# Optimization experiments

Measured on AMD Instinct MI355X. Metric: run time of the kernel, lower is better.

Reference implementation:

```python
import jax, jax.numpy as jnp
import numpy as np

VOCA = 30000
EMB = 128
REGION = 7
RADIUS = REGION // 2
NUM_CLASSES = 20
MAX_LEN = 512
ENTIRE = MAX_LEN - 2 * RADIUS
BATCH = 64


def _uniform(k, shape, lo=-0.01, hi=0.01):
    return jax.random.uniform(k, shape, dtype=jnp.float32, minval=lo, maxval=hi)


def _xavier(k, shape):
    fan_out, fan_in = shape
    lim = float(np.sqrt(6.0 / (fan_in + fan_out)))
    return jax.random.uniform(k, shape, dtype=jnp.float32, minval=-lim, maxval=lim)


def setup_inputs() -> dict:
    key = jax.random.key(0)
    ks = jax.random.split(key, 8)
    train_input = jax.random.randint(ks[0], (BATCH, MAX_LEN), 0, VOCA, dtype=jnp.int64)
    # padding_idx=0 -> row 0 is zero in both tables
    emb_region = _uniform(ks[1], (VOCA, REGION * EMB)).at[0].set(0.0)
    emb_word = _uniform(ks[2], (VOCA, EMB)).at[0].set(0.0)
    W_inter = _uniform(ks[3], (NUM_CLASSES, EMB))
    W_agg1 = _xavier(ks[4], (MAX_LEN * 2, ENTIRE))
    b_agg1 = jnp.zeros((MAX_LEN * 2,), jnp.float32)
    W_agg2 = _xavier(ks[5], (1, MAX_LEN * 2))
    b_agg2 = jnp.zeros((1,), jnp.float32)
    return {
        "train_input": train_input,
        "emb_region": emb_region,
        "emb_word": emb_word,
        "W_inter": W_inter,
        "W_agg1": W_agg1,
        "b_agg1": b_agg1,
        "W_agg2": W_agg2,
        "b_agg2": b_agg2,
    }


def reference(train_input, emb_region, emb_word, W_inter, W_agg1, b_agg1, W_agg2, b_agg2):
    B, L = train_input.shape
    entire = L - 2 * RADIUS
    # region embedding of center tokens -> [B, entire, REGION, EMB]
    trimed = train_input[:, RADIUS:L - RADIUS]
    K = emb_region[trimed].reshape(B, entire, REGION, EMB)
    # sliding-window gather of context tokens -> [B, entire, REGION]
    pos = jnp.arange(entire)[:, None] + jnp.arange(REGION)[None, :]
    E = emb_word[train_input[:, pos]]  # [B, entire, REGION, EMB]
    # elementwise interaction, max over region, relu
    inter = jax.nn.relu(jnp.max(E * K, axis=2))  # [B, entire, EMB]
    # per-class word-level scores -> [B, C, entire]
    inter = jnp.einsum("bne,ce->bcn", inter, W_inter)
    # aggregation MLP over the 'entire' axis (dropout inactive at eval)
    h = jax.nn.relu(inter @ W_agg1.T + b_agg1)  # [B, C, 2*MAX_LEN]
    agreg = (h @ W_agg2.T + b_agg2)[..., 0]  # [B, C]
    prob = jax.nn.softmax(agreg, axis=1)
    class_ = jnp.argmax(prob, axis=1)
    return agreg, prob, class_
```

## Files before the change

### kernel.cpp

```cpp
#include <hip/hip_runtime.h>
#include <math.h>

#define BATCH   64
#define MAXLEN  512
#define EMB     128
#define REGION  7
#define RADIUS  3
#define ENTIRE  506
#define NCLS    20
#define AGG1    1024
#define TILE_N  16
#define ICP     512

__global__ __launch_bounds__(256) void k1_inter(
        const int*   __restrict__ ti,
        const float* __restrict__ embR,
        const float* __restrict__ embW,
        const float* __restrict__ Wint,
        float*       __restrict__ interC) {
    __shared__ float wordbuf[TILE_N + 6][EMB];
    __shared__ float interL[TILE_N][EMB + 1];
    __shared__ float wl[NCLS][EMB + 2];
    __shared__ int   wid[TILE_N + 6];

    const int b   = blockIdx.y;
    const int n0  = blockIdx.x * TILE_N;
    const int np  = min(TILE_N, ENTIRE - n0);
    const int tid = threadIdx.x;

    if (tid < TILE_N + 6) {
        int r = tid;
        wid[r] = (n0 + r < MAXLEN) ? ti[b * MAXLEN + n0 + r] : 0;
    }
    for (int idx = tid; idx < NCLS * EMB; idx += 256) {
        int c = idx >> 7, e = idx & 127;
        wl[c][e] = Wint[idx];
    }
    __syncthreads();

    for (int idx = tid; idx < (TILE_N + 6) * EMB; idx += 256) {
        int r = idx >> 7, e = idx & 127;
        wordbuf[r][e] = embW[(long)wid[r] * EMB + e];
    }
    __syncthreads();

    for (int pp = 0; pp < TILE_N; pp += 2) {
        int p = pp + (tid >> 7);
        int e = tid & 127;
        if (p < np) {
            long t = wid[p + RADIUS];
            const float* kr = embR + t * (REGION * EMB) + e;
            float m = -INFINITY;
            #pragma unroll
            for (int j = 0; j < REGION; ++j) {
                float ew = wordbuf[p + j][e];
                float kk = kr[(long)j * EMB];
                m = fmaxf(m, ew * kk);
            }
            interL[p][e] = fmaxf(m, 0.f);
        }
    }
    __syncthreads();

    for (int out = tid; out < NCLS * TILE_N; out += 256) {
        int c = out >> 4;
        int p = out & 15;
        int n = n0 + p;
        if (p < np) {
            float s = 0.f;
            #pragma unroll 8
            for (int e = 0; e < EMB; ++e)
                s += interL[p][e] * wl[c][e];
            interC[((long)b * NCLS + c) * ICP + n] = s;
        }
    }
}

__global__ __launch_bounds__(256) void k2_gemm(
        const float* __restrict__ interC,
        const float* __restrict__ Wagg1,
        const float* __restrict__ bagg1,
        float*       __restrict__ h) {
    const int n  = blockIdx.x * 256 + threadIdx.x;
    const int m0 = blockIdx.y * 16;

    float acc[16];
    #pragma unroll
    for (int i = 0; i < 16; ++i) acc[i] = 0.f;

    const float2* w2  = (const float2*)Wagg1 + (long)n * (ENTIRE / 2);
    const float*  icb = interC + (long)m0 * ICP;

    for (int kc = 0; kc < 126; ++kc) {
        float2 wa = w2[kc * 2];
        float2 wb = w2[kc * 2 + 1];
        #pragma unroll
        for (int mm = 0; mm < 16; ++mm) {
            float4 ic = *(const float4*)(icb + mm * ICP + kc * 4);
            acc[mm] += ic.x * wa.x + ic.y * wa.y + ic.z * wb.x + ic.w * wb.y;
        }
    }
    {
        float wta = Wagg1[(long)n * ENTIRE + 504];
        float wtb = Wagg1[(long)n * ENTIRE + 505];
        #pragma unroll
        for (int mm = 0; mm < 16; ++mm)
            acc[mm] += icb[mm * ICP + 504] * wta + icb[mm * ICP + 505] * wtb;
    }

    float bias = bagg1[n];
    #pragma unroll
    for (int mm = 0; mm < 16; ++mm)
        h[(long)(m0 + mm) * AGG1 + n] = fmaxf(acc[mm] + bias, 0.f);
}

__global__ __launch_bounds__(256) void k3_agreg(
        const float* __restrict__ h,
        const float* __restrict__ Wagg2,
        const float* __restrict__ bagg2,
        float*       __restrict__ out) {
    const int m    = blockIdx.x * 4 + (threadIdx.x >> 6);
    const int lane = threadIdx.x & 63;
    const float* hr = h + (long)m * AGG1;
    float s = 0.f;
    #pragma unroll
    for (int i = 0; i < AGG1 / 64; ++i)
        s += hr[i * 64 + lane] * Wagg2[i * 64 + lane];
    #pragma unroll
    for (int off = 32; off >= 1; off >>= 1)
        s += __shfl_down(s, off, 64);
    if (lane == 0) out[m] = s + bagg2[0];
}

__global__ void k4_softmax(float* __restrict__ out) {
    int b = threadIdx.x;
    if (b >= BATCH) return;
    float v[NCLS];
    float mx = -INFINITY;
    for (int c = 0; c < NCLS; ++c) {
        v[c] = out[b * NCLS + c];
        mx = fmaxf(mx, v[c]);
    }
    float sum = 0.f;
    for (int c = 0; c < NCLS; ++c) { v[c] = expf(v[c] - mx); sum += v[c]; }
    float inv = 1.f / sum;
    int best = 0; float bv = -INFINITY;
    for (int c = 0; c < NCLS; ++c) {
        float p = v[c] * inv;
        out[BATCH * NCLS + b * NCLS + c] = p;
        if (p > bv) { bv = p; best = c; }
    }
    out[2 * BATCH * NCLS + b] = (float)best;
}

extern "C" void kernel_launch(void* const* d_in, const int* in_sizes, int n_in,
                              void* d_out, int out_size, void* d_ws, size_t ws_size,
                              hipStream_t stream) {
    const int*   ti    = (const int*)  d_in[0];
    const float* embR  = (const float*)d_in[1];
    const float* embW  = (const float*)d_in[2];
    const float* Wint  = (const float*)d_in[3];
    const float* Wagg1 = (const float*)d_in[4];
    const float* bagg1 = (const float*)d_in[5];
    const float* Wagg2 = (const float*)d_in[6];
    const float* bagg2 = (const float*)d_in[7];
    float* out = (float*)d_out;

    float* interC = (float*)d_ws;
    float* h      = interC + (size_t)BATCH * NCLS * ICP;

    k1_inter  <<<dim3((ENTIRE + TILE_N - 1) / TILE_N, BATCH), 256, 0, stream>>>(ti, embR, embW, Wint, interC);
    k2_gemm   <<<dim3(AGG1 / 256, BATCH * NCLS / 16),   256, 0, stream>>>(interC, Wagg1, bagg1, h);
    k3_agreg  <<<BATCH * NCLS / 4,                      256, 0, stream>>>(h, Wagg2, bagg2, out);
    k4_softmax<<<1, 64, 0, stream>>>(out);
}
```

Measured before the change: 288.3 us.

## Tile aggregation GEMM through shared memory and fuse output dot with softmax

The aggregation GEMM now stages 64x64 activation tiles and 32x64 weight tiles in LDS, with each thread computing a 4x2 register tile, instead of every thread streaming weights and activations directly from global memory. The padded interC columns are now written as zeros so the GEMM can read a full K of 512 without a separate tail step. The final dot product with W_agg2 and the softmax/argmax are fused into one per-batch kernel, removing a launch and the single-block softmax. Risks include a smaller per-thread register tile, with more LDS traffic and block syncs per FLOP.

```diff
diff --git a/kernel.cpp b/kernel.cpp
--- a/kernel.cpp
+++ b/kernel.cpp
@@ -44,6 +44,7 @@
     }
     __syncthreads();
 
+    #pragma unroll 4
     for (int pp = 0; pp < TILE_N; pp += 2) {
         int p = pp + (tid >> 7);
         int e = tid & 127;
@@ -62,9 +63,9 @@
     }
     __syncthreads();
 
-    for (int out = tid; out < NCLS * TILE_N; out += 256) {
-        int c = out >> 4;
-        int p = out & 15;
+    for (int oi = tid; oi < NCLS * TILE_N; oi += 256) {
+        int c = oi >> 4;
+        int p = oi & 15;
         int n = n0 + p;
         if (p < np) {
             float s = 0.f;
@@ -72,85 +73,122 @@
             for (int e = 0; e < EMB; ++e)
                 s += interL[p][e] * wl[c][e];
             interC[((long)b * NCLS + c) * ICP + n] = s;
+        } else {
+            interC[((long)b * NCLS + c) * ICP + n] = 0.f;
         }
     }
 }
 
 __global__ __launch_bounds__(256) void k2_gemm(
-        const float* __restrict__ interC,
-        const float* __restrict__ Wagg1,
-        const float* __restrict__ bagg1,
+        const float* __restrict__ ic,
+        const float* __restrict__ W1,
+        const float* __restrict__ b1,
         float*       __restrict__ h) {
-    const int n  = blockIdx.x * 256 + threadIdx.x;
-    const int m0 = blockIdx.y * 16;
-
-    float acc[16];
+    __shared__ float As[64][68];
+    __shared__ float Bs[32][68];
+    const int tid = threadIdx.x;
+    const int n0  = blockIdx.x * 32;
+    const int m0  = blockIdx.y * 64;
+    const int tm  = tid >> 4;
+    const int tn  = tid & 15;
+
+    float acc[4][2] = {{0.f, 0.f}, {0.f, 0.f}, {0.f, 0.f}, {0.f, 0.f}};
+
+    for (int k0 = 0; k0 < 512; k0 += 64) {
+        #pragma unroll
+        for (int r = 0; r < 4; ++r) {
+            int row = r * 16 + tm;
+            *(float4*)&As[row][tn * 4] =
+                *(const float4*)&ic[(size_t)(m0 + row) * ICP + k0 + tn * 4];
+        }
+        #pragma unroll
+        for (int r = 0; r < 2; ++r) {
+            int row = r * 16 + tm;
+            #pragma unroll
+            for (int j = 0; j < 2; ++j) {
+                int col = 2 * tn + 32 * j;
+                int gk  = k0 + col;
+                float2 v = make_float2(0.f, 0.f);
+                if (gk < ENTIRE)
+                    v = *(const float2*)&W1[(size_t)(n0 + row) * ENTIRE + gk];
+                *(float2*)&Bs[row][col] = v;
+            }
+        }
+        __syncthreads();
+
+        #pragma unroll
+        for (int kq = 0; kq < 64; kq += 4) {
+            float4 a[4], bb[2];
+            #pragma unroll
+            for (int i = 0; i < 4; ++i) a[i]  = *(const float4*)&As[tm + 16 * i][kq];
+            #pragma unroll
+            for (int j = 0; j < 2; ++j) bb[j] = *(const float4*)&Bs[tn + 16 * j][kq];
+            #pragma unroll
+            for (int i = 0; i < 4; ++i)
+                #pragma unroll
+                for (int j = 0; j < 2; ++j)
+                    acc[i][j] += a[i].x * bb[j].x + a[i].y * bb[j].y
+                               + a[i].z * bb[j].z + a[i].w * bb[j].w;
+        }
+        __syncthreads();
+    }
+
     #pragma unroll
-    for (int i = 0; i < 16; ++i) acc[i] = 0.f;
-
-    const float2* w2  = (const float2*)Wagg1 + (long)n * (ENTIRE / 2);
-    const float*  icb = interC + (long)m0 * ICP;
-
-    for (int kc = 0; kc < 126; ++kc) {
-        float2 wa = w2[kc * 2];
-        float2 wb = w2[kc * 2 + 1];
-        #pragma unroll
-        for (int mm = 0; mm < 16; ++mm) {
-            float4 ic = *(const float4*)(icb + mm * ICP + kc * 4);
-            acc[mm] += ic.x * wa.x + ic.y * wa.y + ic.z * wb.x + ic.w * wb.y;
-        }
-    }
-    {
-        float wta = Wagg1[(long)n * ENTIRE + 504];
-        float wtb = Wagg1[(long)n * ENTIRE + 505];
-        #pragma unroll
-        for (int mm = 0; mm < 16; ++mm)
-            acc[mm] += icb[mm * ICP + 504] * wta + icb[mm * ICP + 505] * wtb;
-    }
-
-    float bias = bagg1[n];
+    for (int i = 0; i < 4; ++i) {
+        int m = m0 + tm + 16 * i;
+        #pragma unroll
+        for (int j = 0; j < 2; ++j) {
+            int n = n0 + tn + 16 * j;
+            h[(size_t)m * AGG1 + n] = fmaxf(acc[i][j] + b1[n], 0.f);
+        }
+    }
+}
+
+__global__ __launch_bounds__(256) void k3_out(
+        const float* __restrict__ h,
+        const float* __restrict__ W2,
+        const float* __restrict__ b2,
+        float*       __restrict__ out) {
+    __shared__ float w[AGG1];
+    __shared__ float ag[NCLS];
+    const int b    = blockIdx.x;
+    const int tid  = threadIdx.x;
+    const int wv   = tid >> 6;
+    const int lane = tid & 63;
+
     #pragma unroll
-    for (int mm = 0; mm < 16; ++mm)
-        h[(long)(m0 + mm) * AGG1 + n] = fmaxf(acc[mm] + bias, 0.f);
-}
-
-__global__ __launch_bounds__(256) void k3_agreg(
-        const float* __restrict__ h,
-        const float* __restrict__ Wagg2,
-        const float* __restrict__ bagg2,
-        float*       __restrict__ out) {
-    const int m    = blockIdx.x * 4 + (threadIdx.x >> 6);
-    const int lane = threadIdx.x & 63;
-    const float* hr = h + (long)m * AGG1;
-    float s = 0.f;
-    #pragma unroll
-    for (int i = 0; i < AGG1 / 64; ++i)
-        s += hr[i * 64 + lane] * Wagg2[i * 64 + lane];
-    #pragma unroll
-    for (int off = 32; off >= 1; off >>= 1)
-        s += __shfl_down(s, off, 64);
-    if (lane == 0) out[m] = s + bagg2[0];
-}
-
-__global__ void k4_softmax(float* __restrict__ out) {
-    int b = threadIdx.x;
-    if (b >= BATCH) return;
-    float v[NCLS];
-    float mx = -INFINITY;
-    for (int c = 0; c < NCLS; ++c) {
-        v[c] = out[b * NCLS + c];
-        mx = fmaxf(mx, v[c]);
-    }
-    float sum = 0.f;
-    for (int c = 0; c < NCLS; ++c) { v[c] = expf(v[c] - mx); sum += v[c]; }
-    float inv = 1.f / sum;
-    int best = 0; float bv = -INFINITY;
-    for (int c = 0; c < NCLS; ++c) {
-        float p = v[c] * inv;
-        out[BATCH * NCLS + b * NCLS + c] = p;
-        if (p > bv) { bv = p; best = c; }
-    }
-    out[2 * BATCH * NCLS + b] = (float)best;
+    for (int i = 0; i < 4; ++i) w[tid + 256 * i] = W2[tid + 256 * i];
+    __syncthreads();
+
+    for (int c = wv; c < NCLS; c += 4) {
+        const float* hr = h + ((size_t)b * NCLS + c) * AGG1;
+        float s = 0.f;
+        #pragma unroll
+        for (int i = 0; i < AGG1 / 64; ++i)
+            s += hr[i * 64 + lane] * w[i * 64 + lane];
+        #pragma unroll
+        for (int off = 32; off >= 1; off >>= 1)
+            s += __shfl_down(s, off, 64);
+        if (lane == 0) ag[c] = s + b2[0];
+    }
+    __syncthreads();
+
+    if (tid == 0) {
+        float mx = -INFINITY;
+        for (int c = 0; c < NCLS; ++c) mx = fmaxf(mx, ag[c]);
+        float e[NCLS];
+        float sum = 0.f;
+        for (int c = 0; c < NCLS; ++c) { e[c] = expf(ag[c] - mx); sum += e[c]; }
+        float inv = 1.f / sum;
+        int best = 0; float bv = -INFINITY;
+        for (int c = 0; c < NCLS; ++c) {
+            out[b * NCLS + c] = ag[c];
+            float p = e[c] * inv;
+            out[BATCH * NCLS + b * NCLS + c] = p;
+            if (p > bv) { bv = p; best = c; }
+        }
+        out[2 * BATCH * NCLS + b] = (float)best;
+    }
 }
 
 extern "C" void kernel_launch(void* const* d_in, const int* in_sizes, int n_in,
@@ -169,8 +207,9 @@
     float* interC = (float*)d_ws;
     float* h      = interC + (size_t)BATCH * NCLS * ICP;
 
-    k1_inter  <<<dim3((ENTIRE + TILE_N - 1) / TILE_N, BATCH), 256, 0, stream>>>(ti, embR, embW, Wint, interC);
-    k2_gemm   <<<dim3(AGG1 / 256, BATCH * NCLS / 16),   256, 0, stream>>>(interC, Wagg1, bagg1, h);
-    k3_agreg  <<<BATCH * NCLS / 4,                      256, 0, stream>>>(h, Wagg2, bagg2, out);
-    k4_softmax<<<1, 64, 0, stream>>>(out);
-}
+    k1_inter<<<dim3((ENTIRE + TILE_N - 1) / TILE_N, BATCH), 256, 0, stream>>>(
+        ti, embR, embW, Wint, interC);
+    k2_gemm<<<dim3(AGG1 / 32, BATCH * NCLS / 64), 256, 0, stream>>>(
+        interC, Wagg1, bagg1, h);
+    k3_out<<<BATCH, 256, 0, stream>>>(h, Wagg2, bagg2, out);
+}
```

Measured after the change: 250.1 us. 1.15x faster.
